# Performance work log

Hardware: AMD Instinct MI355X
Metric: run time of the kernel (lower is better)

Reference implementation:

```python
import jax, jax.numpy as jnp
import numpy as np

N = 131072   # total utterances (nodes)
B = 2048     # conversations (segments)
F = 200      # n_features (hard-coded 200 in source)
STEPS = 3    # processing_steps (reason_steps[0])


def setup_inputs() -> dict:
    key = jax.random.key(0)
    k = jax.random.split(key, 8)
    x = jax.random.normal(k[0], (N, F), dtype=jnp.float32)
    batch = jnp.sort(jax.random.randint(k[1], (N,), 0, B, dtype=jnp.int32))
    cos_coef = jax.random.normal(k[2], (N,), dtype=jnp.float32)
    q_star = jax.random.normal(k[3], (B, 2 * F), dtype=jnp.float32)
    s = 1.0 / np.sqrt(F)
    # PyTorch LSTM params: gate order i, f, g, o; input size 2F, hidden F
    W_ih = jax.random.uniform(k[4], (4 * F, 2 * F), jnp.float32, -s, s)
    W_hh = jax.random.uniform(k[5], (4 * F, F), jnp.float32, -s, s)
    b_ih = jax.random.uniform(k[6], (4 * F,), jnp.float32, -s, s)
    b_hh = jax.random.uniform(k[7], (4 * F,), jnp.float32, -s, s)
    return {"x": x, "batch": batch, "cos_coef": cos_coef, "q_star": q_star,
            "W_ih": W_ih, "W_hh": W_hh, "b_ih": b_ih, "b_hh": b_hh}


def _lstm_cell(inp, h, c, W_ih, W_hh, b_ih, b_hh):
    gates = inp @ W_ih.T + b_ih + h @ W_hh.T + b_hh  # [B, 4F]
    i, f, g, o = jnp.split(gates, 4, axis=-1)
    c = jax.nn.sigmoid(f) * c + jax.nn.sigmoid(i) * jnp.tanh(g)
    h = jax.nn.sigmoid(o) * jnp.tanh(c)
    return h, c


def reference(x, batch, cos_coef, q_star, W_ih, W_hh, b_ih, b_hh):
    # initial LSTM hidden: a_sit[i] = cos_row_i @ x[segment_i]  -> segment_sum
    h = jax.ops.segment_sum(cos_coef[:, None] * x, batch, num_segments=B)  # [B,F]
    c = jnp.zeros((B, F), dtype=x.dtype)
    for _ in range(STEPS):
        h, c = _lstm_cell(q_star, h, c, W_ih, W_hh, b_ih, b_hh)
        q = h                                            # [B,F]
        e = jnp.sum(x * q[batch], axis=-1)               # [N]
        m = jax.ops.segment_max(e, batch, num_segments=B)
        ex = jnp.exp(e - m[batch])
        denom = jax.ops.segment_sum(ex, batch, num_segments=B)
        a = ex / denom[batch]                            # per-segment softmax
        r = jax.ops.segment_sum(a[:, None] * x, batch, num_segments=B)  # [B,F]
        q_star = jnp.concatenate([q, r], axis=-1)        # [B,2F]
    return q_star
```

## Files before the change

### kernel.cpp

```cpp
#include <hip/hip_runtime.h>
#include <hip/hip_bf16.h>

#define N_NODES 131072
#define B_SEG   2048
#define F_DIM   200
#define K_DIM   608
#define MAXSEG  128

typedef __attribute__((ext_vector_type(8))) short bf16x8;
typedef __attribute__((ext_vector_type(4))) float f32x4;

__device__ __forceinline__ float b2f(unsigned short u) {
  union { unsigned int i; float f; } v; v.i = ((unsigned int)u) << 16; return v.f;
}
__device__ __forceinline__ unsigned short f2bu(float f) {
  __hip_bfloat16 h = __float2bfloat16(f);
  return *reinterpret_cast<unsigned short*>(&h);
}
__device__ __forceinline__ float sigmoidf_(float x) { return 1.f / (1.f + __expf(-x)); }

__global__ __launch_bounds__(256) void setup_kernel(
    const float* __restrict__ Wih, const float* __restrict__ Whh,
    const float* __restrict__ bih, const float* __restrict__ bhh,
    const int* __restrict__ batch, unsigned short* __restrict__ Wc,
    float* __restrict__ bsum, int* __restrict__ seg_off) {
  int bid = blockIdx.x, tid = threadIdx.x;
  if (bid < 1976) {
    int idx = bid * 256 + tid;
    int row = idx / K_DIM, k = idx - row * K_DIM;
    float v = 0.f;
    if (row < 800) {
      if (k < 400)      v = Wih[row * 400 + k];
      else if (k < 600) v = Whh[row * 200 + (k - 400)];
    }
    Wc[idx] = f2bu(v);
  } else if (bid < 1976 + 512) {
    int i = (bid - 1976) * 256 + tid;
    int v  = batch[i];
    int pv = (i == 0) ? -1 : batch[i - 1];
    for (int b = pv + 1; b <= v; b++) seg_off[b] = i;
  } else {
    int idx = (bid - 2488) * 256 + tid;
    if (idx < 800) bsum[idx] = bih[idx] + bhh[idx];
    else if (idx == 800) {
      int last = batch[N_NODES - 1];
      for (int b = last + 1; b <= B_SEG; b++) seg_off[b] = N_NODES;
    }
  }
}

__global__ __launch_bounds__(256) void init_kernel(
    const float* __restrict__ xf, const int* __restrict__ seg_off,
    const float* __restrict__ cosc, const float* __restrict__ qs0,
    unsigned short* __restrict__ xb, unsigned short* __restrict__ A) {
  __shared__ float rpart[4][F_DIM];
  int b = blockIdx.x, tid = threadIdx.x;
  int start = seg_off[b], end = seg_off[b + 1];
  int n = end - start;
  unsigned short* Arow = A + (size_t)b * K_DIM;
  int wave = tid >> 6, lane = tid & 63;
  float a0 = 0.f, a1 = 0.f, a2 = 0.f, a3 = 0.f;
  for (int r = wave; r < n; r += 4) {
    if (lane < 50) {
      float4 v = *(const float4*)(xf + (size_t)(start + r) * F_DIM + 4 * lane);
      ushort4 o; o.x = f2bu(v.x); o.y = f2bu(v.y); o.z = f2bu(v.z); o.w = f2bu(v.w);
      *(ushort4*)(xb + (size_t)(start + r) * F_DIM + 4 * lane) = o;
      float cv = cosc[start + r];
      a0 += cv * b2f(o.x); a1 += cv * b2f(o.y);
      a2 += cv * b2f(o.z); a3 += cv * b2f(o.w);
    }
  }
  if (lane < 50) {
    rpart[wave][4 * lane]     = a0;
    rpart[wave][4 * lane + 1] = a1;
    rpart[wave][4 * lane + 2] = a2;
    rpart[wave][4 * lane + 3] = a3;
  }
  for (int j = tid; j < 400; j += 256)
    Arow[j] = f2bu(qs0[(size_t)b * 400 + j]);
  if (tid < 8) Arow[600 + tid] = 0;
  __syncthreads();
  if (tid < F_DIM) {
    float acc = rpart[0][tid] + rpart[1][tid] + rpart[2][tid] + rpart[3][tid];
    Arow[400 + tid] = f2bu(acc);
  }
}

__global__ __launch_bounds__(256) void gemm_gates(
    const unsigned short* __restrict__ A, const unsigned short* __restrict__ W,
    float* __restrict__ gates) {
  int tid = threadIdx.x;
  int bm = blockIdx.x * 64, bn = blockIdx.y * 64;
  int wave = tid >> 6, lane = tid & 63;
  int quad = lane >> 4, col = lane & 15;
  f32x4 acc[4];
#pragma unroll
  for (int t = 0; t < 4; t++) acc[t] = (f32x4){0.f, 0.f, 0.f, 0.f};
  const unsigned short* Ap = A + (size_t)(bm + wave * 16 + col) * K_DIM + quad * 8;
  const unsigned short* Wp = W + (size_t)(bn + col) * K_DIM + quad * 8;
#pragma unroll
  for (int k0 = 0; k0 < K_DIM; k0 += 32) {
    bf16x8 af = *(const bf16x8*)(Ap + k0);
#pragma unroll
    for (int t = 0; t < 4; t++) {
      bf16x8 bfr = *(const bf16x8*)(Wp + (size_t)t * 16 * K_DIM + k0);
      acc[t] = __builtin_amdgcn_mfma_f32_16x16x32_bf16(af, bfr, acc[t], 0, 0, 0);
    }
  }
#pragma unroll
  for (int t = 0; t < 4; t++) {
    int gn = bn + t * 16 + col;
    if (gn < 800) {
#pragma unroll
      for (int r = 0; r < 4; r++) {
        int gm = bm + wave * 16 + quad * 4 + r;
        gates[(size_t)gm * 800 + gn] = acc[t][r];
      }
    }
  }
}

__global__ __launch_bounds__(256) void attn_fused(
    const unsigned short* __restrict__ xb, const int* __restrict__ seg_off,
    const float* __restrict__ gates, const float* __restrict__ bsum,
    float* __restrict__ cvec, float* __restrict__ esc,
    unsigned short* __restrict__ A, float* __restrict__ out, int step) {
  __shared__ float e_s[MAXSEG];
  __shared__ float q_s[F_DIM];
  __shared__ float rpart[4][F_DIM];
  __shared__ float red[8];
  int b = blockIdx.x, tid = threadIdx.x;
  int start = seg_off[b], end = seg_off[b + 1];
  int n = end - start;
  bool small = (n <= MAXSEG);
  float* e_arr = small ? e_s : (esc + start);
  unsigned short* Arow = A + (size_t)b * K_DIM;
  if (tid < F_DIM) {
    int f = tid;
    const float* g = gates + (size_t)b * 800;
    float gi = g[f]       + bsum[f];
    float gf = g[200 + f] + bsum[200 + f];
    float gg = g[400 + f] + bsum[400 + f];
    float go = g[600 + f] + bsum[600 + f];
    float cp = (step > 0) ? cvec[(size_t)b * F_DIM + f] : 0.f;
    float cn = sigmoidf_(gf) * cp + sigmoidf_(gi) * tanhf(gg);
    float hn = sigmoidf_(go) * tanhf(cn);
    cvec[(size_t)b * F_DIM + f] = cn;
    q_s[f] = hn;
    if (step < 2) {
      unsigned short hb = f2bu(hn);
      Arow[f] = hb;
      Arow[400 + f] = hb;
    }
  }
  __syncthreads();
  int wave = tid >> 6, lane = tid & 63;
  float q0 = 0.f, q1 = 0.f, q2 = 0.f, q3 = 0.f;
  if (lane < 50) {
    q0 = q_s[4 * lane];     q1 = q_s[4 * lane + 1];
    q2 = q_s[4 * lane + 2]; q3 = q_s[4 * lane + 3];
  }
  const unsigned short* xrow = xb + (size_t)start * F_DIM + 4 * lane;
  for (int r = wave; r < n; r += 4) {
    float p = 0.f;
    if (lane < 50) {
      ushort4 v = *(const ushort4*)(xrow + (size_t)r * F_DIM);
      p = q0 * b2f(v.x) + q1 * b2f(v.y) + q2 * b2f(v.z) + q3 * b2f(v.w);
    }
#pragma unroll
    for (int off = 32; off; off >>= 1) p += __shfl_down(p, off);
    if (lane == 0) e_arr[r] = p;
  }
  __syncthreads();
  float pm = -3.4e38f;
  for (int i = tid; i < n; i += 256) pm = fmaxf(pm, e_arr[i]);
#pragma unroll
  for (int off = 32; off; off >>= 1) pm = fmaxf(pm, __shfl_down(pm, off));
  if (lane == 0) red[wave] = pm;
  __syncthreads();
  float m = fmaxf(fmaxf(red[0], red[1]), fmaxf(red[2], red[3]));
  float ps = 0.f;
  for (int i = tid; i < n; i += 256) {
    float ex = __expf(e_arr[i] - m);
    e_arr[i] = ex;
    ps += ex;
  }
#pragma unroll
  for (int off = 32; off; off >>= 1) ps += __shfl_down(ps, off);
  if (lane == 0) red[4 + wave] = ps;
  __syncthreads();
  float denom = red[4] + red[5] + red[6] + red[7];
  float inv = (denom > 0.f) ? 1.f / denom : 0.f;
  float a0 = 0.f, a1 = 0.f, a2 = 0.f, a3 = 0.f;
  for (int r = wave; r < n; r += 4) {
    float wv = e_arr[r];
    if (lane < 50) {
      ushort4 v = *(const ushort4*)(xrow + (size_t)r * F_DIM);
      a0 += wv * b2f(v.x); a1 += wv * b2f(v.y);
      a2 += wv * b2f(v.z); a3 += wv * b2f(v.w);
    }
  }
  if (lane < 50) {
    rpart[wave][4 * lane]     = a0;
    rpart[wave][4 * lane + 1] = a1;
    rpart[wave][4 * lane + 2] = a2;
    rpart[wave][4 * lane + 3] = a3;
  }
  __syncthreads();
  if (tid < F_DIM) {
    float rv = (rpart[0][tid] + rpart[1][tid] + rpart[2][tid] + rpart[3][tid]) * inv;
    if (step < 2) {
      Arow[200 + tid] = f2bu(rv);
    } else {
      out[(size_t)b * 400 + tid]       = q_s[tid];
      out[(size_t)b * 400 + 200 + tid] = rv;
    }
  }
}

extern "C" void kernel_launch(void* const* d_in, const int* in_sizes, int n_in,
                              void* d_out, int out_size, void* d_ws, size_t ws_size,
                              hipStream_t stream) {
  const float* x    = (const float*)d_in[0];
  const int*   batch= (const int*)d_in[1];
  const float* cosc = (const float*)d_in[2];
  const float* qs0  = (const float*)d_in[3];
  const float* Wih  = (const float*)d_in[4];
  const float* Whh  = (const float*)d_in[5];
  const float* bih  = (const float*)d_in[6];
  const float* bhh  = (const float*)d_in[7];
  char* ws = (char*)d_ws;
  unsigned short* xb   = (unsigned short*)(ws);
  unsigned short* A    = (unsigned short*)(ws + 52428800);
  unsigned short* Wc   = (unsigned short*)(ws + 54919168);
  float*          gates= (float*)(ws + 55930880);
  float*          cvec = (float*)(ws + 62484480);
  float*          bsum = (float*)(ws + 64122880);
  int*            soff = (int*)(ws + 64126080);
  float*          esc  = (float*)(ws + 64134288);
  float*          outp = (float*)d_out;

  setup_kernel<<<2492, 256, 0, stream>>>(Wih, Whh, bih, bhh, batch, Wc, bsum, soff);
  init_kernel<<<B_SEG, 256, 0, stream>>>(x, soff, cosc, qs0, xb, A);
  for (int s = 0; s < 3; s++) {
    gemm_gates<<<dim3(32, 13), 256, 0, stream>>>(A, Wc, gates);
    attn_fused<<<B_SEG, 256, 0, stream>>>(xb, soff, gates, bsum, cvec, esc, A, outp, s);
  }
}
```

Baseline: 306.7 us.

## Use single-pass online softmax in attention to read x once

```diff
diff --git a/kernel.cpp b/kernel.cpp
--- a/kernel.cpp
+++ b/kernel.cpp
@@ -5,7 +5,7 @@
 #define B_SEG   2048
 #define F_DIM   200
 #define K_DIM   608
-#define MAXSEG  128
+#define NEG_INF (-3.4e38f)
 
 typedef __attribute__((ext_vector_type(8))) short bf16x8;
 typedef __attribute__((ext_vector_type(4))) float f32x4;
@@ -123,17 +123,14 @@
 __global__ __launch_bounds__(256) void attn_fused(
     const unsigned short* __restrict__ xb, const int* __restrict__ seg_off,
     const float* __restrict__ gates, const float* __restrict__ bsum,
-    float* __restrict__ cvec, float* __restrict__ esc,
-    unsigned short* __restrict__ A, float* __restrict__ out, int step) {
-  __shared__ float e_s[MAXSEG];
+    float* __restrict__ cvec, unsigned short* __restrict__ A,
+    float* __restrict__ out, int step) {
   __shared__ float q_s[F_DIM];
   __shared__ float rpart[4][F_DIM];
   __shared__ float red[8];
   int b = blockIdx.x, tid = threadIdx.x;
   int start = seg_off[b], end = seg_off[b + 1];
   int n = end - start;
-  bool small = (n <= MAXSEG);
-  float* e_arr = small ? e_s : (esc + start);
   unsigned short* Arow = A + (size_t)b * K_DIM;
   if (tid < F_DIM) {
     int f = tid;
@@ -161,52 +158,41 @@
     q2 = q_s[4 * lane + 2]; q3 = q_s[4 * lane + 3];
   }
   const unsigned short* xrow = xb + (size_t)start * F_DIM + 4 * lane;
+  float m = NEG_INF, l = 0.f;
+  float a0 = 0.f, a1 = 0.f, a2 = 0.f, a3 = 0.f;
   for (int r = wave; r < n; r += 4) {
+    float x0 = 0.f, x1 = 0.f, x2 = 0.f, x3 = 0.f;
     float p = 0.f;
     if (lane < 50) {
       ushort4 v = *(const ushort4*)(xrow + (size_t)r * F_DIM);
-      p = q0 * b2f(v.x) + q1 * b2f(v.y) + q2 * b2f(v.z) + q3 * b2f(v.w);
+      x0 = b2f(v.x); x1 = b2f(v.y); x2 = b2f(v.z); x3 = b2f(v.w);
+      p = q0 * x0 + q1 * x1 + q2 * x2 + q3 * x3;
     }
 #pragma unroll
     for (int off = 32; off; off >>= 1) p += __shfl_down(p, off);
-    if (lane == 0) e_arr[r] = p;
-  }
-  __syncthreads();
-  float pm = -3.4e38f;
-  for (int i = tid; i < n; i += 256) pm = fmaxf(pm, e_arr[i]);
-#pragma unroll
-  for (int off = 32; off; off >>= 1) pm = fmaxf(pm, __shfl_down(pm, off));
-  if (lane == 0) red[wave] = pm;
-  __syncthreads();
-  float m = fmaxf(fmaxf(red[0], red[1]), fmaxf(red[2], red[3]));
-  float ps = 0.f;
-  for (int i = tid; i < n; i += 256) {
-    float ex = __expf(e_arr[i] - m);
-    e_arr[i] = ex;
-    ps += ex;
-  }
-#pragma unroll
-  for (int off = 32; off; off >>= 1) ps += __shfl_down(ps, off);
-  if (lane == 0) red[4 + wave] = ps;
-  __syncthreads();
-  float denom = red[4] + red[5] + red[6] + red[7];
-  float inv = (denom > 0.f) ? 1.f / denom : 0.f;
-  float a0 = 0.f, a1 = 0.f, a2 = 0.f, a3 = 0.f;
-  for (int r = wave; r < n; r += 4) {
-    float wv = e_arr[r];
-    if (lane < 50) {
-      ushort4 v = *(const ushort4*)(xrow + (size_t)r * F_DIM);
-      a0 += wv * b2f(v.x); a1 += wv * b2f(v.y);
-      a2 += wv * b2f(v.z); a3 += wv * b2f(v.w);
-    }
-  }
+    float e = __shfl(p, 0);
+    float mn = fmaxf(m, e);
+    float fac = __expf(m - mn);
+    float w  = __expf(e - mn);
+    l  = l * fac + w;
+    a0 = a0 * fac + w * x0;  a1 = a1 * fac + w * x1;
+    a2 = a2 * fac + w * x2;  a3 = a3 * fac + w * x3;
+    m = mn;
+  }
+  if (lane == 0) red[wave] = m;
+  __syncthreads();
+  float M = fmaxf(fmaxf(red[0], red[1]), fmaxf(red[2], red[3]));
+  float facw = (m > NEG_INF) ? __expf(m - M) : 0.f;
+  if (lane == 0) red[4 + wave] = l * facw;
   if (lane < 50) {
-    rpart[wave][4 * lane]     = a0;
-    rpart[wave][4 * lane + 1] = a1;
-    rpart[wave][4 * lane + 2] = a2;
-    rpart[wave][4 * lane + 3] = a3;
-  }
-  __syncthreads();
+    rpart[wave][4 * lane]     = a0 * facw;
+    rpart[wave][4 * lane + 1] = a1 * facw;
+    rpart[wave][4 * lane + 2] = a2 * facw;
+    rpart[wave][4 * lane + 3] = a3 * facw;
+  }
+  __syncthreads();
+  float L = red[4] + red[5] + red[6] + red[7];
+  float inv = (L > 0.f) ? 1.f / L : 0.f;
   if (tid < F_DIM) {
     float rv = (rpart[0][tid] + rpart[1][tid] + rpart[2][tid] + rpart[3][tid]) * inv;
     if (step < 2) {
@@ -237,13 +223,12 @@
   float*          cvec = (float*)(ws + 62484480);
   float*          bsum = (float*)(ws + 64122880);
   int*            soff = (int*)(ws + 64126080);
-  float*          esc  = (float*)(ws + 64134288);
   float*          outp = (float*)d_out;
 
   setup_kernel<<<2492, 256, 0, stream>>>(Wih, Whh, bih, bhh, batch, Wc, bsum, soff);
   init_kernel<<<B_SEG, 256, 0, stream>>>(x, soff, cosc, qs0, xb, A);
   for (int s = 0; s < 3; s++) {
     gemm_gates<<<dim3(32, 13), 256, 0, stream>>>(A, Wc, gates);
-    attn_fused<<<B_SEG, 256, 0, stream>>>(xb, soff, gates, bsum, cvec, esc, A, outp, s);
-  }
-}
+    attn_fused<<<B_SEG, 256, 0, stream>>>(xb, soff, gates, bsum, cvec, A, outp, s);
+  }
+}
```

After: 287.9 us. 6.1% less time.
